# Optimization experiments

Hardware: AMD Instinct MI355X
Metric: run time of the kernel (lower is better)

The kernel has to match this reference:

```python
import jax, jax.numpy as jnp
import numpy as np

N, D, E = 50000, 128, 800000
EPS = 1e-5


def setup_inputs() -> dict:
    key = jax.random.key(0)
    ks = jax.random.split(key, 16)
    x = jax.random.normal(ks[0], (N, D), dtype=jnp.float32)
    edge_index = jax.random.randint(ks[1], (2, E), 0, N, dtype=jnp.int32)
    s = 1.0 / np.sqrt(D)
    inp = {"x": x, "edge_index": edge_index}
    for i in range(3):
        inp[f"lng{i}"] = jnp.ones((D,), jnp.float32)
        inp[f"lnb{i}"] = jnp.zeros((D,), jnp.float32)
        inp[f"W{i}"] = jax.random.normal(ks[2 + 2 * i], (D, D), jnp.float32) * s
        inp[f"b{i}"] = jnp.zeros((D,), jnp.float32)
    return inp


def _gcn_norm(edge_index):
    # PyG GCNConv default: add self loops, symmetric normalization D^-1/2 (A+I) D^-1/2
    loop = jnp.arange(N, dtype=edge_index.dtype)
    src = jnp.concatenate([edge_index[0], loop])  # [E+N]
    dst = jnp.concatenate([edge_index[1], loop])
    deg = jax.ops.segment_sum(jnp.ones_like(dst, jnp.float32), dst, num_segments=N)
    dinv = jnp.where(deg > 0, jax.lax.rsqrt(jnp.maximum(deg, 1.0)), 0.0)
    norm = dinv[src] * dinv[dst]  # [E+N]
    return src, dst, norm


def _layer(h, g, bt, W, b, src, dst, norm):
    # LayerNorm -> ReLU -> GCNConv
    mu = jnp.mean(h, axis=-1, keepdims=True)
    var = jnp.mean(jnp.square(h - mu), axis=-1, keepdims=True)
    hn = (h - mu) * jax.lax.rsqrt(var + EPS) * g + bt
    hn = jax.nn.relu(hn) @ W  # [N, D]
    msg = norm[:, None] * hn[src]  # [E+N, D] gather
    return jax.ops.segment_sum(msg, dst, num_segments=N) + b


def reference(x, edge_index, lng0, lnb0, W0, b0, lng1, lnb1, W1, b1, lng2, lnb2, W2, b2):
    src, dst, norm = _gcn_norm(edge_index)
    # conv0 (GCNLayer) + residual
    x = _layer(x, lng0, lnb0, W0, b0, src, dst, norm) + x
    # conv1 (ResGCNLayer: two GCNLayers) + residual
    h = _layer(x, lng1, lnb1, W1, b1, src, dst, norm)
    h = _layer(h, lng2, lnb2, W2, b2, src, dst, norm)
    return h + x
```

## Files before the change

### kernel.cpp

```cpp
#include <hip/hip_runtime.h>

#define N_NODES 50000
#define DIM     128
#define E_EDGES 800000
#define ELLW    64

typedef __attribute__((ext_vector_type(8))) short short8;
typedef __attribute__((ext_vector_type(4))) float f32x4;

__device__ __forceinline__ float bflo(unsigned int u){ return __uint_as_float(u << 16); }
__device__ __forceinline__ float bfhi(unsigned int u){ return __uint_as_float(u & 0xFFFF0000u); }
__device__ __forceinline__ unsigned int f2bf(float f){
  unsigned int u = __float_as_uint(f);
  return (u + 0x7FFFu + ((u >> 16) & 1u)) >> 16;
}
__device__ __forceinline__ unsigned int pack2(float a, float b){
  return f2bf(a) | (f2bf(b) << 16);
}


__global__ __launch_bounds__(256) void count_kernel(const int* __restrict__ edges,
                                                    int* __restrict__ cnt,
                                                    int* __restrict__ epos){
  int e = blockIdx.x * 256 + threadIdx.x;
  if (e < E_EDGES) epos[e] = atomicAdd(&cnt[edges[E_EDGES + e]], 1);
}

__global__ __launch_bounds__(256) void fill_kernel(const int* __restrict__ edges,
                                                   const int* __restrict__ epos,
                                                   const int* __restrict__ cnt,
                                                   int2* __restrict__ ell){
  int e = blockIdx.x * 256 + threadIdx.x;
  if (e < E_EDGES){
    int s = edges[e];
    int d = edges[E_EDGES + e];
    int pos = epos[e];
    if (pos < ELLW){
      float w = rsqrtf((float)(cnt[s] + 1)) * rsqrtf((float)(cnt[d] + 1));
      int2 pk; pk.x = s; pk.y = __float_as_int(w);
      ell[(size_t)d * ELLW + pos] = pk;
    }
  }
}

__global__ __launch_bounds__(256) void cvtw_all(const float* __restrict__ W0,
                                                const float* __restrict__ W1,
                                                const float* __restrict__ W2,
                                                unsigned short* __restrict__ Wt){
  int idx = blockIdx.x * 256 + threadIdx.x;
  int w = idx >> 14, r = idx & 16383;
  const float* W = (w == 0) ? W0 : (w == 1) ? W1 : W2;
  int k = r >> 7, n = r & 127;
  Wt[w * 16384 + n * 128 + k] = (unsigned short)f2bf(W[r]);
}


__global__ __launch_bounds__(256) void gemm_ln_mfma(const float* __restrict__ X,
                                                    const float* __restrict__ g,
                                                    const float* __restrict__ bt,
                                                    const unsigned short* __restrict__ Wt,
                                                    unsigned short* __restrict__ Y){
  __shared__ unsigned short ldsb[128 * 136];
  int tid = threadIdx.x;
  #pragma unroll
  for (int it = 0; it < 8; ++it){
    int c  = tid + it * 256;
    int n  = c >> 4, kc = c & 15;
    *(short8*)&ldsb[n * 136 + kc * 8] = *(const short8*)(Wt + n * 128 + kc * 8);
  }
  int wave = tid >> 6, lane = tid & 63, quad = lane >> 4, l15 = lane & 15;
  int rowbase = blockIdx.x * 128 + wave * 32;
  int rm0 = rowbase + l15;      if (rm0 > N_NODES - 1) rm0 = N_NODES - 1;
  int rm1 = rowbase + 16 + l15; if (rm1 > N_NODES - 1) rm1 = N_NODES - 1;

  float v0[4][8], v1[4][8];
  float s0 = 0.f, ss0 = 0.f, s1 = 0.f, ss1 = 0.f;
  #pragma unroll
  for (int kk = 0; kk < 4; ++kk){
    float4 xa = *(const float4*)(X + (size_t)rm0 * 128 + kk * 32 + quad * 8);
    float4 xb = *(const float4*)(X + (size_t)rm0 * 128 + kk * 32 + quad * 8 + 4);
    float4 ya = *(const float4*)(X + (size_t)rm1 * 128 + kk * 32 + quad * 8);
    float4 yb_ = *(const float4*)(X + (size_t)rm1 * 128 + kk * 32 + quad * 8 + 4);
    v0[kk][0]=xa.x; v0[kk][1]=xa.y; v0[kk][2]=xa.z; v0[kk][3]=xa.w;
    v0[kk][4]=xb.x; v0[kk][5]=xb.y; v0[kk][6]=xb.z; v0[kk][7]=xb.w;
    v1[kk][0]=ya.x; v1[kk][1]=ya.y; v1[kk][2]=ya.z; v1[kk][3]=ya.w;
    v1[kk][4]=yb_.x; v1[kk][5]=yb_.y; v1[kk][6]=yb_.z; v1[kk][7]=yb_.w;
    #pragma unroll
    for (int j = 0; j < 8; ++j){
      s0 += v0[kk][j]; ss0 += v0[kk][j] * v0[kk][j];
      s1 += v1[kk][j]; ss1 += v1[kk][j] * v1[kk][j];
    }
  }
  s0 += __shfl_xor(s0, 16, 64); ss0 += __shfl_xor(ss0, 16, 64);
  s0 += __shfl_xor(s0, 32, 64); ss0 += __shfl_xor(ss0, 32, 64);
  s1 += __shfl_xor(s1, 16, 64); ss1 += __shfl_xor(ss1, 16, 64);
  s1 += __shfl_xor(s1, 32, 64); ss1 += __shfl_xor(ss1, 32, 64);
  float mu0 = s0 * (1.0f/128.0f), var0 = ss0 * (1.0f/128.0f) - mu0*mu0;
  float mu1 = s1 * (1.0f/128.0f), var1 = ss1 * (1.0f/128.0f) - mu1*mu1;
  float rs0 = rsqrtf(var0 + 1e-5f), rs1 = rsqrtf(var1 + 1e-5f);

  short8 a0[4], a1[4];
  #pragma unroll
  for (int kk = 0; kk < 4; ++kk){
    float4 ga = *(const float4*)(g  + kk * 32 + quad * 8);
    float4 gb = *(const float4*)(g  + kk * 32 + quad * 8 + 4);
    float4 ba = *(const float4*)(bt + kk * 32 + quad * 8);
    float4 bb = *(const float4*)(bt + kk * 32 + quad * 8 + 4);
    float gg[8] = {ga.x,ga.y,ga.z,ga.w,gb.x,gb.y,gb.z,gb.w};
    float bbv[8] = {ba.x,ba.y,ba.z,ba.w,bb.x,bb.y,bb.z,bb.w};
    #pragma unroll
    for (int j = 0; j < 8; ++j){
      float h0 = fmaxf((v0[kk][j] - mu0) * rs0 * gg[j] + bbv[j], 0.0f);
      float h1 = fmaxf((v1[kk][j] - mu1) * rs1 * gg[j] + bbv[j], 0.0f);
      a0[kk][j] = (short)f2bf(h0);
      a1[kk][j] = (short)f2bf(h1);
    }
  }

  f32x4 acc[2][8];
  #pragma unroll
  for (int mt = 0; mt < 2; ++mt)
    #pragma unroll
    for (int nt = 0; nt < 8; ++nt) acc[mt][nt] = (f32x4){0.f, 0.f, 0.f, 0.f};
  __syncthreads();
  #pragma unroll
  for (int kk = 0; kk < 4; ++kk){
    #pragma unroll
    for (int nt = 0; nt < 8; ++nt){
      short8 b = *(const short8*)&ldsb[(nt * 16 + l15) * 136 + kk * 32 + quad * 8];
      acc[0][nt] = __builtin_amdgcn_mfma_f32_16x16x32_bf16(a0[kk], b, acc[0][nt], 0, 0, 0);
      acc[1][nt] = __builtin_amdgcn_mfma_f32_16x16x32_bf16(a1[kk], b, acc[1][nt], 0, 0, 0);
    }
  }
  #pragma unroll
  for (int mt = 0; mt < 2; ++mt)
    #pragma unroll
    for (int nt = 0; nt < 8; ++nt)
      #pragma unroll
      for (int r = 0; r < 4; ++r){
        int row = rowbase + mt * 16 + quad * 4 + r;
        if (row < N_NODES)
          Y[(size_t)row * 128 + nt * 16 + l15] = (unsigned short)f2bf(acc[mt][nt][r]);
      }
}


__global__ __launch_bounds__(256) void gemm_mfma(const unsigned short* __restrict__ A,
                                                 const unsigned short* __restrict__ Wt,
                                                 unsigned short* __restrict__ Y){
  __shared__ unsigned short ldsb[128 * 136];
  int tid = threadIdx.x;
  #pragma unroll
  for (int it = 0; it < 8; ++it){
    int c  = tid + it * 256;
    int n  = c >> 4, kc = c & 15;
    *(short8*)&ldsb[n * 136 + kc * 8] = *(const short8*)(Wt + n * 128 + kc * 8);
  }
  int wave = tid >> 6, lane = tid & 63, quad = lane >> 4, l15 = lane & 15;
  int rowbase = blockIdx.x * 128 + wave * 32;
  int rm0 = rowbase + l15;      if (rm0 > N_NODES - 1) rm0 = N_NODES - 1;
  int rm1 = rowbase + 16 + l15; if (rm1 > N_NODES - 1) rm1 = N_NODES - 1;

  short8 a0[4], a1[4];
  #pragma unroll
  for (int kk = 0; kk < 4; ++kk){
    a0[kk] = *(const short8*)(A + (size_t)rm0 * 128 + kk * 32 + quad * 8);
    a1[kk] = *(const short8*)(A + (size_t)rm1 * 128 + kk * 32 + quad * 8);
  }
  f32x4 acc[2][8];
  #pragma unroll
  for (int mt = 0; mt < 2; ++mt)
    #pragma unroll
    for (int nt = 0; nt < 8; ++nt) acc[mt][nt] = (f32x4){0.f, 0.f, 0.f, 0.f};
  __syncthreads();
  #pragma unroll
  for (int kk = 0; kk < 4; ++kk){
    #pragma unroll
    for (int nt = 0; nt < 8; ++nt){
      short8 b = *(const short8*)&ldsb[(nt * 16 + l15) * 136 + kk * 32 + quad * 8];
      acc[0][nt] = __builtin_amdgcn_mfma_f32_16x16x32_bf16(a0[kk], b, acc[0][nt], 0, 0, 0);
      acc[1][nt] = __builtin_amdgcn_mfma_f32_16x16x32_bf16(a1[kk], b, acc[1][nt], 0, 0, 0);
    }
  }
  #pragma unroll
  for (int mt = 0; mt < 2; ++mt)
    #pragma unroll
    for (int nt = 0; nt < 8; ++nt)
      #pragma unroll
      for (int r = 0; r < 4; ++r){
        int row = rowbase + mt * 16 + quad * 4 + r;
        if (row < N_NODES)
          Y[(size_t)row * 128 + nt * 16 + l15] = (unsigned short)f2bf(acc[mt][nt][r]);
      }
}


template<bool HAS_RES, bool DO_LN>
__global__ __launch_bounds__(256) void agg_kernel(const unsigned short* __restrict__ y,
                                                  const int* __restrict__ cnt,
                                                  const int2* __restrict__ ell,
                                                  const float* __restrict__ bias,
                                                  const float* __restrict__ res,
                                                  float* __restrict__ outp,
                                                  const float* __restrict__ lng,
                                                  const float* __restrict__ lnb,
                                                  unsigned short* __restrict__ hn_out){
  int wv   = (blockIdx.x * 256 + threadIdx.x) >> 6;
  int lane = threadIdx.x & 63;
  int hl   = lane & 15;
  int node = wv * 4 + (lane >> 4);
  int selbase = lane & 48;
  const uint4* y4 = (const uint4*)y;

  int deg = cnt[node];
  float di = rsqrtf((float)(deg + 1));
  float ws = di * di;

  const int2* row = ell + (size_t)node * ELLW;
  int2 e0 = row[hl], e1 = row[hl + 16], e2 = row[hl + 32], e3 = row[hl + 48];

  int J = deg;
  J = max(J, __shfl_xor(J, 16, 64));
  J = max(J, __shfl_xor(J, 32, 64));

  uint4 us = y4[(size_t)node * 16 + hl];
  float acc0 = ws * bflo(us.x), acc1 = ws * bfhi(us.x);
  float acc2 = ws * bflo(us.y), acc3 = ws * bfhi(us.y);
  float acc4 = ws * bflo(us.z), acc5 = ws * bfhi(us.z);
  float acc6 = ws * bflo(us.w), acc7 = ws * bfhi(us.w);

  auto block16 = [&](int2 ee, int base16){
    int rem = J - base16;
    if (rem <= 0) return;
    int nch = (min(rem, 16) + 3) >> 2;
    for (int c = 0; c < nch; ++c){
      int rb = c * 4;
      int sA = __shfl(ee.x, selbase | (rb + 0), 64);
      int sB = __shfl(ee.x, selbase | (rb + 1), 64);
      int sC = __shfl(ee.x, selbase | (rb + 2), 64);
      int sD = __shfl(ee.x, selbase | (rb + 3), 64);
      float wA = __uint_as_float((unsigned)__shfl(ee.y, selbase | (rb + 0), 64));
      float wB = __uint_as_float((unsigned)__shfl(ee.y, selbase | (rb + 1), 64));
      float wC = __uint_as_float((unsigned)__shfl(ee.y, selbase | (rb + 2), 64));
      float wD = __uint_as_float((unsigned)__shfl(ee.y, selbase | (rb + 3), 64));
      uint4 gA = y4[(size_t)sA * 16 + hl];
      uint4 gB = y4[(size_t)sB * 16 + hl];
      uint4 gC = y4[(size_t)sC * 16 + hl];
      uint4 gD = y4[(size_t)sD * 16 + hl];
      acc0 += wA*bflo(gA.x); acc1 += wA*bfhi(gA.x); acc2 += wA*bflo(gA.y); acc3 += wA*bfhi(gA.y);
      acc4 += wA*bflo(gA.z); acc5 += wA*bfhi(gA.z); acc6 += wA*bflo(gA.w); acc7 += wA*bfhi(gA.w);
      acc0 += wB*bflo(gB.x); acc1 += wB*bfhi(gB.x); acc2 += wB*bflo(gB.y); acc3 += wB*bfhi(gB.y);
      acc4 += wB*bflo(gB.z); acc5 += wB*bfhi(gB.z); acc6 += wB*bflo(gB.w); acc7 += wB*bfhi(gB.w);
      acc0 += wC*bflo(gC.x); acc1 += wC*bfhi(gC.x); acc2 += wC*bflo(gC.y); acc3 += wC*bfhi(gC.y);
      acc4 += wC*bflo(gC.z); acc5 += wC*bfhi(gC.z); acc6 += wC*bflo(gC.w); acc7 += wC*bfhi(gC.w);
      acc0 += wD*bflo(gD.x); acc1 += wD*bfhi(gD.x); acc2 += wD*bflo(gD.y); acc3 += wD*bfhi(gD.y);
      acc4 += wD*bflo(gD.z); acc5 += wD*bfhi(gD.z); acc6 += wD*bflo(gD.w); acc7 += wD*bfhi(gD.w);
    }
  };
  block16(e0, 0); block16(e1, 16); block16(e2, 32); block16(e3, 48);

  float4 ubA = ((const float4*)bias)[hl * 2];
  float4 ubB = ((const float4*)bias)[hl * 2 + 1];
  acc0 += ubA.x; acc1 += ubA.y; acc2 += ubA.z; acc3 += ubA.w;
  acc4 += ubB.x; acc5 += ubB.y; acc6 += ubB.z; acc7 += ubB.w;
  if (HAS_RES){
    float4 urA = ((const float4*)res)[(size_t)node * 32 + hl * 2];
    float4 urB = ((const float4*)res)[(size_t)node * 32 + hl * 2 + 1];
    acc0 += urA.x; acc1 += urA.y; acc2 += urA.z; acc3 += urA.w;
    acc4 += urB.x; acc5 += urB.y; acc6 += urB.z; acc7 += urB.w;
  }
  if (outp){
    float4 oA; oA.x = acc0; oA.y = acc1; oA.z = acc2; oA.w = acc3;
    float4 oB; oB.x = acc4; oB.y = acc5; oB.z = acc6; oB.w = acc7;
    ((float4*)outp)[(size_t)node * 32 + hl * 2]     = oA;
    ((float4*)outp)[(size_t)node * 32 + hl * 2 + 1] = oB;
  }

  if (DO_LN){
    float s  = acc0 + acc1 + acc2 + acc3 + acc4 + acc5 + acc6 + acc7;
    float ss = acc0*acc0 + acc1*acc1 + acc2*acc2 + acc3*acc3
             + acc4*acc4 + acc5*acc5 + acc6*acc6 + acc7*acc7;
    #pragma unroll
    for (int d = 8; d >= 1; d >>= 1){ s += __shfl_xor(s, d, 64); ss += __shfl_xor(ss, d, 64); }
    float mu  = s * (1.0f / 128.0f);
    float var = ss * (1.0f / 128.0f) - mu * mu;
    float rs  = rsqrtf(var + 1e-5f);
    float4 ugA = ((const float4*)lng)[hl * 2];
    float4 ugB = ((const float4*)lng)[hl * 2 + 1];
    float4 ubbA = ((const float4*)lnb)[hl * 2];
    float4 ubbB = ((const float4*)lnb)[hl * 2 + 1];
    float h0 = fmaxf((acc0 - mu) * rs * ugA.x + ubbA.x, 0.0f);
    float h1 = fmaxf((acc1 - mu) * rs * ugA.y + ubbA.y, 0.0f);
    float h2 = fmaxf((acc2 - mu) * rs * ugA.z + ubbA.z, 0.0f);
    float h3 = fmaxf((acc3 - mu) * rs * ugA.w + ubbA.w, 0.0f);
    float h4 = fmaxf((acc4 - mu) * rs * ugB.x + ubbB.x, 0.0f);
    float h5 = fmaxf((acc5 - mu) * rs * ugB.y + ubbB.y, 0.0f);
    float h6 = fmaxf((acc6 - mu) * rs * ugB.z + ubbB.z, 0.0f);
    float h7 = fmaxf((acc7 - mu) * rs * ugB.w + ubbB.w, 0.0f);
    uint4 ho;
    ho.x = pack2(h0, h1); ho.y = pack2(h2, h3);
    ho.z = pack2(h4, h5); ho.w = pack2(h6, h7);
    ((uint4*)hn_out)[(size_t)node * 16 + hl] = ho;
  }
}


extern "C" void kernel_launch(void* const* d_in, const int* in_sizes, int n_in,
                              void* d_out, int out_size, void* d_ws, size_t ws_size,
                              hipStream_t stream){
  const float* x    = (const float*)d_in[0];
  const int*   edges= (const int*)d_in[1];
  const float* lng0 = (const float*)d_in[2];
  const float* lnb0 = (const float*)d_in[3];
  const float* W0   = (const float*)d_in[4];
  const float* b0   = (const float*)d_in[5];
  const float* lng1 = (const float*)d_in[6];
  const float* lnb1 = (const float*)d_in[7];
  const float* W1   = (const float*)d_in[8];
  const float* b1   = (const float*)d_in[9];
  const float* lng2 = (const float*)d_in[10];
  const float* lnb2 = (const float*)d_in[11];
  const float* W2   = (const float*)d_in[12];
  const float* b2   = (const float*)d_in[13];

  char* p = (char*)d_ws;
  auto carve = [&](size_t bytes) -> void* {
    void* r = (void*)p;
    p += (bytes + 255) & ~(size_t)255;
    return r;
  };
  int*   cnt   = (int*)  carve(N_NODES * 4);
  int2*  ell   = (int2*) carve((size_t)N_NODES * ELLW * 8);
  size_t zspan = (char*)(ell + (size_t)N_NODES * ELLW) - (char*)cnt;
  int*   epos  = (int*)  carve((size_t)E_EDGES * 4);
  unsigned short* Wt = (unsigned short*)carve(3 * 128 * 128 * 2);
  unsigned short* hn = (unsigned short*)carve((size_t)N_NODES * 128 * 2);
  unsigned short* yb = (unsigned short*)carve((size_t)N_NODES * 128 * 2);
  float* out = (float*)d_out;

  hipMemsetAsync(cnt, 0, zspan, stream);

  count_kernel<<<(E_EDGES + 255) / 256, 256, 0, stream>>>(edges, cnt, epos);
  fill_kernel<<<(E_EDGES + 255) / 256, 256, 0, stream>>>(edges, epos, cnt, ell);
  cvtw_all<<<192, 256, 0, stream>>>(W0, W1, W2, Wt);

  const int GEMM_GRID = (N_NODES + 127) / 128;
  const int AGG_GRID  = N_NODES / 4 / 4;

  gemm_ln_mfma<<<GEMM_GRID, 256, 0, stream>>>(x, lng0, lnb0, Wt, yb);
  agg_kernel<true, true><<<AGG_GRID, 256, 0, stream>>>(yb, cnt, ell,
                                                       b0, x, out, lng1, lnb1, hn);
  gemm_mfma<<<GEMM_GRID, 256, 0, stream>>>(hn, Wt + 16384, yb);
  agg_kernel<false, true><<<AGG_GRID, 256, 0, stream>>>(yb, cnt, ell,
                                                        b1, nullptr, nullptr, lng2, lnb2, hn);
  gemm_mfma<<<GEMM_GRID, 256, 0, stream>>>(hn, Wt + 32768, yb);
  agg_kernel<true, false><<<AGG_GRID, 256, 0, stream>>>(yb, cnt, ell,
                                                        b2, out, out, nullptr, nullptr, nullptr);
}
```

Baseline: 300.3 us.

## Fuse all GCN stages into one persistent cooperative kernel with grid syncs

```diff
diff --git a/kernel.cpp b/kernel.cpp
--- a/kernel.cpp
+++ b/kernel.cpp
@@ -1,4 +1,7 @@
 #include <hip/hip_runtime.h>
+#include <hip/hip_cooperative_groups.h>
+
+namespace cg = cooperative_groups;
 
 #define N_NODES 50000
 #define DIM     128
@@ -18,310 +21,329 @@
   return f2bf(a) | (f2bf(b) << 16);
 }
 
-
-__global__ __launch_bounds__(256) void count_kernel(const int* __restrict__ edges,
-                                                    int* __restrict__ cnt,
-                                                    int* __restrict__ epos){
-  int e = blockIdx.x * 256 + threadIdx.x;
-  if (e < E_EDGES) epos[e] = atomicAdd(&cnt[edges[E_EDGES + e]], 1);
-}
-
-__global__ __launch_bounds__(256) void fill_kernel(const int* __restrict__ edges,
-                                                   const int* __restrict__ epos,
-                                                   const int* __restrict__ cnt,
-                                                   int2* __restrict__ ell){
-  int e = blockIdx.x * 256 + threadIdx.x;
-  if (e < E_EDGES){
-    int s = edges[e];
-    int d = edges[E_EDGES + e];
-    int pos = epos[e];
-    if (pos < ELLW){
-      float w = rsqrtf((float)(cnt[s] + 1)) * rsqrtf((float)(cnt[d] + 1));
-      int2 pk; pk.x = s; pk.y = __float_as_int(w);
-      ell[(size_t)d * ELLW + pos] = pk;
-    }
-  }
-}
-
-__global__ __launch_bounds__(256) void cvtw_all(const float* __restrict__ W0,
-                                                const float* __restrict__ W1,
-                                                const float* __restrict__ W2,
-                                                unsigned short* __restrict__ Wt){
-  int idx = blockIdx.x * 256 + threadIdx.x;
-  int w = idx >> 14, r = idx & 16383;
-  const float* W = (w == 0) ? W0 : (w == 1) ? W1 : W2;
-  int k = r >> 7, n = r & 127;
-  Wt[w * 16384 + n * 128 + k] = (unsigned short)f2bf(W[r]);
-}
-
-
-__global__ __launch_bounds__(256) void gemm_ln_mfma(const float* __restrict__ X,
-                                                    const float* __restrict__ g,
-                                                    const float* __restrict__ bt,
-                                                    const unsigned short* __restrict__ Wt,
-                                                    unsigned short* __restrict__ Y){
-  __shared__ unsigned short ldsb[128 * 136];
-  int tid = threadIdx.x;
-  #pragma unroll
-  for (int it = 0; it < 8; ++it){
-    int c  = tid + it * 256;
-    int n  = c >> 4, kc = c & 15;
-    *(short8*)&ldsb[n * 136 + kc * 8] = *(const short8*)(Wt + n * 128 + kc * 8);
-  }
-  int wave = tid >> 6, lane = tid & 63, quad = lane >> 4, l15 = lane & 15;
-  int rowbase = blockIdx.x * 128 + wave * 32;
-  int rm0 = rowbase + l15;      if (rm0 > N_NODES - 1) rm0 = N_NODES - 1;
-  int rm1 = rowbase + 16 + l15; if (rm1 > N_NODES - 1) rm1 = N_NODES - 1;
-
-  float v0[4][8], v1[4][8];
-  float s0 = 0.f, ss0 = 0.f, s1 = 0.f, ss1 = 0.f;
+struct Params {
+  const float* x; const int* edges;
+  const float* lng0; const float* lnb0; const float* W0; const float* b0;
+  const float* lng1; const float* lnb1; const float* W1; const float* b1;
+  const float* lng2; const float* lnb2; const float* W2; const float* b2;
+  int* cnt; int* epos; int2* ell; unsigned short* Wt;
+  unsigned short* hn; unsigned short* yb; float* out;
+};
+
+__device__ __forceinline__ void gemm_tile(const unsigned short* __restrict__ A,
+                                          const unsigned short* __restrict__ ldsb,
+                                          unsigned short* __restrict__ Y,
+                                          int base, int wave, int quad, int l15){
+  int rbase = base + wave * 16;
+  int rm = rbase + l15; if (rm > N_NODES - 1) rm = N_NODES - 1;
+  short8 a[4];
+  #pragma unroll
+  for (int kk = 0; kk < 4; ++kk)
+    a[kk] = *(const short8*)(A + (size_t)rm * 128 + kk * 32 + quad * 8);
+  f32x4 acc[8];
+  #pragma unroll
+  for (int nt = 0; nt < 8; ++nt) acc[nt] = (f32x4){0.f, 0.f, 0.f, 0.f};
+  #pragma unroll
+  for (int kk = 0; kk < 4; ++kk)
+    #pragma unroll
+    for (int nt = 0; nt < 8; ++nt){
+      short8 b = *(const short8*)&ldsb[(nt * 16 + l15) * 136 + kk * 32 + quad * 8];
+      acc[nt] = __builtin_amdgcn_mfma_f32_16x16x32_bf16(a[kk], b, acc[nt], 0, 0, 0);
+    }
+  #pragma unroll
+  for (int nt = 0; nt < 8; ++nt)
+    #pragma unroll
+    for (int r = 0; r < 4; ++r){
+      int row = rbase + quad * 4 + r;
+      if (row < N_NODES)
+        Y[(size_t)row * 128 + nt * 16 + l15] = (unsigned short)f2bf(acc[nt][r]);
+    }
+}
+
+__device__ __forceinline__ void gemm_ln_tile(const float* __restrict__ X,
+                                             const float* __restrict__ g,
+                                             const float* __restrict__ bt,
+                                             const unsigned short* __restrict__ ldsb,
+                                             unsigned short* __restrict__ Y,
+                                             int base, int wave, int quad, int l15){
+  int rbase = base + wave * 16;
+  int rm = rbase + l15; if (rm > N_NODES - 1) rm = N_NODES - 1;
+  float v[4][8];
+  float s = 0.f, ss = 0.f;
   #pragma unroll
   for (int kk = 0; kk < 4; ++kk){
-    float4 xa = *(const float4*)(X + (size_t)rm0 * 128 + kk * 32 + quad * 8);
-    float4 xb = *(const float4*)(X + (size_t)rm0 * 128 + kk * 32 + quad * 8 + 4);
-    float4 ya = *(const float4*)(X + (size_t)rm1 * 128 + kk * 32 + quad * 8);
-    float4 yb_ = *(const float4*)(X + (size_t)rm1 * 128 + kk * 32 + quad * 8 + 4);
-    v0[kk][0]=xa.x; v0[kk][1]=xa.y; v0[kk][2]=xa.z; v0[kk][3]=xa.w;
-    v0[kk][4]=xb.x; v0[kk][5]=xb.y; v0[kk][6]=xb.z; v0[kk][7]=xb.w;
-    v1[kk][0]=ya.x; v1[kk][1]=ya.y; v1[kk][2]=ya.z; v1[kk][3]=ya.w;
-    v1[kk][4]=yb_.x; v1[kk][5]=yb_.y; v1[kk][6]=yb_.z; v1[kk][7]=yb_.w;
-    #pragma unroll
-    for (int j = 0; j < 8; ++j){
-      s0 += v0[kk][j]; ss0 += v0[kk][j] * v0[kk][j];
-      s1 += v1[kk][j]; ss1 += v1[kk][j] * v1[kk][j];
-    }
-  }
-  s0 += __shfl_xor(s0, 16, 64); ss0 += __shfl_xor(ss0, 16, 64);
-  s0 += __shfl_xor(s0, 32, 64); ss0 += __shfl_xor(ss0, 32, 64);
-  s1 += __shfl_xor(s1, 16, 64); ss1 += __shfl_xor(ss1, 16, 64);
-  s1 += __shfl_xor(s1, 32, 64); ss1 += __shfl_xor(ss1, 32, 64);
-  float mu0 = s0 * (1.0f/128.0f), var0 = ss0 * (1.0f/128.0f) - mu0*mu0;
-  float mu1 = s1 * (1.0f/128.0f), var1 = ss1 * (1.0f/128.0f) - mu1*mu1;
-  float rs0 = rsqrtf(var0 + 1e-5f), rs1 = rsqrtf(var1 + 1e-5f);
-
-  short8 a0[4], a1[4];
+    float4 xa = *(const float4*)(X + (size_t)rm * 128 + kk * 32 + quad * 8);
+    float4 xb = *(const float4*)(X + (size_t)rm * 128 + kk * 32 + quad * 8 + 4);
+    v[kk][0]=xa.x; v[kk][1]=xa.y; v[kk][2]=xa.z; v[kk][3]=xa.w;
+    v[kk][4]=xb.x; v[kk][5]=xb.y; v[kk][6]=xb.z; v[kk][7]=xb.w;
+    #pragma unroll
+    for (int j = 0; j < 8; ++j){ s += v[kk][j]; ss += v[kk][j] * v[kk][j]; }
+  }
+  s += __shfl_xor(s, 16, 64); ss += __shfl_xor(ss, 16, 64);
+  s += __shfl_xor(s, 32, 64); ss += __shfl_xor(ss, 32, 64);
+  float mu = s * (1.0f/128.0f), var = ss * (1.0f/128.0f) - mu * mu;
+  float rs = rsqrtf(var + 1e-5f);
+  short8 a[4];
   #pragma unroll
   for (int kk = 0; kk < 4; ++kk){
     float4 ga = *(const float4*)(g  + kk * 32 + quad * 8);
     float4 gb = *(const float4*)(g  + kk * 32 + quad * 8 + 4);
     float4 ba = *(const float4*)(bt + kk * 32 + quad * 8);
     float4 bb = *(const float4*)(bt + kk * 32 + quad * 8 + 4);
-    float gg[8] = {ga.x,ga.y,ga.z,ga.w,gb.x,gb.y,gb.z,gb.w};
+    float gg[8]  = {ga.x,ga.y,ga.z,ga.w,gb.x,gb.y,gb.z,gb.w};
     float bbv[8] = {ba.x,ba.y,ba.z,ba.w,bb.x,bb.y,bb.z,bb.w};
     #pragma unroll
     for (int j = 0; j < 8; ++j){
-      float h0 = fmaxf((v0[kk][j] - mu0) * rs0 * gg[j] + bbv[j], 0.0f);
-      float h1 = fmaxf((v1[kk][j] - mu1) * rs1 * gg[j] + bbv[j], 0.0f);
-      a0[kk][j] = (short)f2bf(h0);
-      a1[kk][j] = (short)f2bf(h1);
-    }
-  }
-
-  f32x4 acc[2][8];
-  #pragma unroll
-  for (int mt = 0; mt < 2; ++mt)
-    #pragma unroll
-    for (int nt = 0; nt < 8; ++nt) acc[mt][nt] = (f32x4){0.f, 0.f, 0.f, 0.f};
-  __syncthreads();
-  #pragma unroll
-  for (int kk = 0; kk < 4; ++kk){
+      float h = fmaxf((v[kk][j] - mu) * rs * gg[j] + bbv[j], 0.0f);
+      a[kk][j] = (short)f2bf(h);
+    }
+  }
+  f32x4 acc[8];
+  #pragma unroll
+  for (int nt = 0; nt < 8; ++nt) acc[nt] = (f32x4){0.f, 0.f, 0.f, 0.f};
+  #pragma unroll
+  for (int kk = 0; kk < 4; ++kk)
     #pragma unroll
     for (int nt = 0; nt < 8; ++nt){
       short8 b = *(const short8*)&ldsb[(nt * 16 + l15) * 136 + kk * 32 + quad * 8];
-      acc[0][nt] = __builtin_amdgcn_mfma_f32_16x16x32_bf16(a0[kk], b, acc[0][nt], 0, 0, 0);
-      acc[1][nt] = __builtin_amdgcn_mfma_f32_16x16x32_bf16(a1[kk], b, acc[1][nt], 0, 0, 0);
-    }
-  }
-  #pragma unroll
-  for (int mt = 0; mt < 2; ++mt)
-    #pragma unroll
-    for (int nt = 0; nt < 8; ++nt)
+      acc[nt] = __builtin_amdgcn_mfma_f32_16x16x32_bf16(a[kk], b, acc[nt], 0, 0, 0);
+    }
+  #pragma unroll
+  for (int nt = 0; nt < 8; ++nt)
+    #pragma unroll
+    for (int r = 0; r < 4; ++r){
+      int row = rbase + quad * 4 + r;
+      if (row < N_NODES)
+        Y[(size_t)row * 128 + nt * 16 + l15] = (unsigned short)f2bf(acc[nt][r]);
+    }
+}
+
+template<bool HAS_RES, bool DO_LN>
+__device__ __forceinline__ void agg_phase(const Params& P,
+                                          const unsigned short* __restrict__ y,
+                                          const float* __restrict__ bias,
+                                          const float* __restrict__ res,
+                                          float* __restrict__ outp,
+                                          const float* __restrict__ lng,
+                                          const float* __restrict__ lnb,
+                                          unsigned short* __restrict__ hn_out,
+                                          int GB){
+  int tid = threadIdx.x, lane = tid & 63, wave = tid >> 6;
+  int hl = lane & 15, selbase = lane & 48;
+  const uint4* y4 = (const uint4*)y;
+  for (int u = blockIdx.x; u < 3125; u += GB){
+    int node = u * 16 + wave * 4 + (lane >> 4);
+    int deg = P.cnt[node];
+    float di = rsqrtf((float)(deg + 1));
+    float ws = di * di;
+
+    const int2* row = P.ell + (size_t)node * ELLW;
+    int2 e0 = row[hl], e1 = row[hl + 16], e2 = row[hl + 32], e3 = row[hl + 48];
+
+    int J = deg;
+    J = max(J, __shfl_xor(J, 16, 64));
+    J = max(J, __shfl_xor(J, 32, 64));
+
+    uint4 us = y4[(size_t)node * 16 + hl];
+    float acc0 = ws * bflo(us.x), acc1 = ws * bfhi(us.x);
+    float acc2 = ws * bflo(us.y), acc3 = ws * bfhi(us.y);
+    float acc4 = ws * bflo(us.z), acc5 = ws * bfhi(us.z);
+    float acc6 = ws * bflo(us.w), acc7 = ws * bfhi(us.w);
+
+    auto block16 = [&](int2 ee, int base16){
+      int rem = J - base16;
+      if (rem <= 0) return;
+      int nch = (min(rem, 16) + 3) >> 2;
+      for (int c = 0; c < nch; ++c){
+        int rb = c * 4;
+        int sA = __shfl(ee.x, selbase | (rb + 0), 64);
+        int sB = __shfl(ee.x, selbase | (rb + 1), 64);
+        int sC = __shfl(ee.x, selbase | (rb + 2), 64);
+        int sD = __shfl(ee.x, selbase | (rb + 3), 64);
+        float wA = __uint_as_float((unsigned)__shfl(ee.y, selbase | (rb + 0), 64));
+        float wB = __uint_as_float((unsigned)__shfl(ee.y, selbase | (rb + 1), 64));
+        float wC = __uint_as_float((unsigned)__shfl(ee.y, selbase | (rb + 2), 64));
+        float wD = __uint_as_float((unsigned)__shfl(ee.y, selbase | (rb + 3), 64));
+        uint4 gA = y4[(size_t)sA * 16 + hl];
+        uint4 gB = y4[(size_t)sB * 16 + hl];
+        uint4 gC = y4[(size_t)sC * 16 + hl];
+        uint4 gD = y4[(size_t)sD * 16 + hl];
+        acc0 += wA*bflo(gA.x); acc1 += wA*bfhi(gA.x); acc2 += wA*bflo(gA.y); acc3 += wA*bfhi(gA.y);
+        acc4 += wA*bflo(gA.z); acc5 += wA*bfhi(gA.z); acc6 += wA*bflo(gA.w); acc7 += wA*bfhi(gA.w);
+        acc0 += wB*bflo(gB.x); acc1 += wB*bfhi(gB.x); acc2 += wB*bflo(gB.y); acc3 += wB*bfhi(gB.y);
+        acc4 += wB*bflo(gB.z); acc5 += wB*bfhi(gB.z); acc6 += wB*bflo(gB.w); acc7 += wB*bfhi(gB.w);
+        acc0 += wC*bflo(gC.x); acc1 += wC*bfhi(gC.x); acc2 += wC*bflo(gC.y); acc3 += wC*bfhi(gC.y);
+        acc4 += wC*bflo(gC.z); acc5 += wC*bfhi(gC.z); acc6 += wC*bflo(gC.w); acc7 += wC*bfhi(gC.w);
+        acc0 += wD*bflo(gD.x); acc1 += wD*bfhi(gD.x); acc2 += wD*bflo(gD.y); acc3 += wD*bfhi(gD.y);
+        acc4 += wD*bflo(gD.z); acc5 += wD*bfhi(gD.z); acc6 += wD*bflo(gD.w); acc7 += wD*bfhi(gD.w);
+      }
+    };
+    block16(e0, 0); block16(e1, 16); block16(e2, 32); block16(e3, 48);
+
+    float4 ubA = ((const float4*)bias)[hl * 2];
+    float4 ubB = ((const float4*)bias)[hl * 2 + 1];
+    acc0 += ubA.x; acc1 += ubA.y; acc2 += ubA.z; acc3 += ubA.w;
+    acc4 += ubB.x; acc5 += ubB.y; acc6 += ubB.z; acc7 += ubB.w;
+    if (HAS_RES){
+      float4 urA = ((const float4*)res)[(size_t)node * 32 + hl * 2];
+      float4 urB = ((const float4*)res)[(size_t)node * 32 + hl * 2 + 1];
+      acc0 += urA.x; acc1 += urA.y; acc2 += urA.z; acc3 += urA.w;
+      acc4 += urB.x; acc5 += urB.y; acc6 += urB.z; acc7 += urB.w;
+    }
+    if (outp){
+      float4 oA; oA.x = acc0; oA.y = acc1; oA.z = acc2; oA.w = acc3;
+      float4 oB; oB.x = acc4; oB.y = acc5; oB.z = acc6; oB.w = acc7;
+      ((float4*)outp)[(size_t)node * 32 + hl * 2]     = oA;
+      ((float4*)outp)[(size_t)node * 32 + hl * 2 + 1] = oB;
+    }
+    if (DO_LN){
+      float s  = acc0 + acc1 + acc2 + acc3 + acc4 + acc5 + acc6 + acc7;
+      float ss = acc0*acc0 + acc1*acc1 + acc2*acc2 + acc3*acc3
+               + acc4*acc4 + acc5*acc5 + acc6*acc6 + acc7*acc7;
       #pragma unroll
-      for (int r = 0; r < 4; ++r){
-        int row = rowbase + mt * 16 + quad * 4 + r;
-        if (row < N_NODES)
-          Y[(size_t)row * 128 + nt * 16 + l15] = (unsigned short)f2bf(acc[mt][nt][r]);
+      for (int d = 8; d >= 1; d >>= 1){ s += __shfl_xor(s, d, 64); ss += __shfl_xor(ss, d, 64); }
+      float mu  = s * (1.0f / 128.0f);
+      float var = ss * (1.0f / 128.0f) - mu * mu;
+      float rs  = rsqrtf(var + 1e-5f);
+      float4 ugA = ((const float4*)lng)[hl * 2];
+      float4 ugB = ((const float4*)lng)[hl * 2 + 1];
+      float4 ubbA = ((const float4*)lnb)[hl * 2];
+      float4 ubbB = ((const float4*)lnb)[hl * 2 + 1];
+      float h0 = fmaxf((acc0 - mu) * rs * ugA.x + ubbA.x, 0.0f);
+      float h1 = fmaxf((acc1 - mu) * rs * ugA.y + ubbA.y, 0.0f);
+      float h2 = fmaxf((acc2 - mu) * rs * ugA.z + ubbA.z, 0.0f);
+      float h3 = fmaxf((acc3 - mu) * rs * ugA.w + ubbA.w, 0.0f);
+      float h4 = fmaxf((acc4 - mu) * rs * ugB.x + ubbB.x, 0.0f);
+      float h5 = fmaxf((acc5 - mu) * rs * ugB.y + ubbB.y, 0.0f);
+      float h6 = fmaxf((acc6 - mu) * rs * ugB.z + ubbB.z, 0.0f);
+      float h7 = fmaxf((acc7 - mu) * rs * ugB.w + ubbB.w, 0.0f);
+      uint4 ho;
+      ho.x = pack2(h0, h1); ho.y = pack2(h2, h3);
+      ho.z = pack2(h4, h5); ho.w = pack2(h6, h7);
+      ((uint4*)hn_out)[(size_t)node * 16 + hl] = ho;
+    }
+  }
+}
+
+
+__global__ __launch_bounds__(256, 4) void mono_kernel(Params P){
+  cg::grid_group grid = cg::this_grid();
+  __shared__ unsigned short ldsb[128 * 136];
+  const int GB   = gridDim.x;
+  const int tid  = threadIdx.x;
+  const int wave = tid >> 6, lane = tid & 63;
+  const int quad = lane >> 4, l15 = lane & 15;
+
+  for (int u = blockIdx.x; u < 196; u += GB){
+    int i = u * 256 + tid;
+    if (i < N_NODES) P.cnt[i] = 0;
+  }
+  grid.sync();
+
+  {
+    const int NU_CNT = 3125, NU_CVT = 192;
+    for (int u = blockIdx.x; u < NU_CNT + NU_CVT; u += GB){
+      if (u < NU_CNT){
+        int e = u * 256 + tid;
+        if (e < E_EDGES) P.epos[e] = atomicAdd(&P.cnt[P.edges[E_EDGES + e]], 1);
+      } else {
+        int idx = (u - NU_CNT) * 256 + tid;
+        int w = idx >> 14, r = idx & 16383;
+        const float* W = (w == 0) ? P.W0 : (w == 1) ? P.W1 : P.W2;
+        P.Wt[w * 16384 + (r & 127) * 128 + (r >> 7)] = (unsigned short)f2bf(W[r]);
       }
-}
-
-
-__global__ __launch_bounds__(256) void gemm_mfma(const unsigned short* __restrict__ A,
-                                                 const unsigned short* __restrict__ Wt,
-                                                 unsigned short* __restrict__ Y){
-  __shared__ unsigned short ldsb[128 * 136];
-  int tid = threadIdx.x;
-  #pragma unroll
-  for (int it = 0; it < 8; ++it){
-    int c  = tid + it * 256;
-    int n  = c >> 4, kc = c & 15;
-    *(short8*)&ldsb[n * 136 + kc * 8] = *(const short8*)(Wt + n * 128 + kc * 8);
-  }
-  int wave = tid >> 6, lane = tid & 63, quad = lane >> 4, l15 = lane & 15;
-  int rowbase = blockIdx.x * 128 + wave * 32;
-  int rm0 = rowbase + l15;      if (rm0 > N_NODES - 1) rm0 = N_NODES - 1;
-  int rm1 = rowbase + 16 + l15; if (rm1 > N_NODES - 1) rm1 = N_NODES - 1;
-
-  short8 a0[4], a1[4];
-  #pragma unroll
-  for (int kk = 0; kk < 4; ++kk){
-    a0[kk] = *(const short8*)(A + (size_t)rm0 * 128 + kk * 32 + quad * 8);
-    a1[kk] = *(const short8*)(A + (size_t)rm1 * 128 + kk * 32 + quad * 8);
-  }
-  f32x4 acc[2][8];
-  #pragma unroll
-  for (int mt = 0; mt < 2; ++mt)
-    #pragma unroll
-    for (int nt = 0; nt < 8; ++nt) acc[mt][nt] = (f32x4){0.f, 0.f, 0.f, 0.f};
-  __syncthreads();
-  #pragma unroll
-  for (int kk = 0; kk < 4; ++kk){
-    #pragma unroll
-    for (int nt = 0; nt < 8; ++nt){
-      short8 b = *(const short8*)&ldsb[(nt * 16 + l15) * 136 + kk * 32 + quad * 8];
-      acc[0][nt] = __builtin_amdgcn_mfma_f32_16x16x32_bf16(a0[kk], b, acc[0][nt], 0, 0, 0);
-      acc[1][nt] = __builtin_amdgcn_mfma_f32_16x16x32_bf16(a1[kk], b, acc[1][nt], 0, 0, 0);
-    }
-  }
-  #pragma unroll
-  for (int mt = 0; mt < 2; ++mt)
-    #pragma unroll
-    for (int nt = 0; nt < 8; ++nt)
-      #pragma unroll
-      for (int r = 0; r < 4; ++r){
-        int row = rowbase + mt * 16 + quad * 4 + r;
-        if (row < N_NODES)
-          Y[(size_t)row * 128 + nt * 16 + l15] = (unsigned short)f2bf(acc[mt][nt][r]);
+    }
+  }
+  grid.sync();
+
+  {
+    #pragma unroll
+    for (int it = 0; it < 8; ++it){
+      int c = tid + it * 256;
+      int n = c >> 4, kc = c & 15;
+      *(short8*)&ldsb[n * 136 + kc * 8] = *(const short8*)(P.Wt + n * 128 + kc * 8);
+    }
+    __syncthreads();
+    const int NU_FILL = 3125, NU_PAD = 196, NU_G = 782;
+    for (int u = blockIdx.x; u < NU_FILL + NU_PAD + NU_G; u += GB){
+      if (u < NU_FILL){
+        int e = u * 256 + tid;
+        if (e < E_EDGES){
+          int s = P.edges[e], d = P.edges[E_EDGES + e];
+          int pos = P.epos[e];
+          if (pos < ELLW){
+            float w = rsqrtf((float)(P.cnt[s] + 1)) * rsqrtf((float)(P.cnt[d] + 1));
+            int2 pk; pk.x = s; pk.y = __float_as_int(w);
+            P.ell[(size_t)d * ELLW + pos] = pk;
+          }
+        }
+      } else if (u < NU_FILL + NU_PAD){
+        int i = (u - NU_FILL) * 256 + tid;
+        if (i < N_NODES){
+          int deg = P.cnt[i];
+          int g4 = (i >> 2) << 2;
+          int J = max(max(P.cnt[g4], P.cnt[g4 + 1]), max(P.cnt[g4 + 2], P.cnt[g4 + 3]));
+          int J4 = min(ELLW, (J + 3) & ~3);
+          int2 z; z.x = 0; z.y = 0;
+          for (int pp = min(deg, J4); pp < J4; ++pp)
+            P.ell[(size_t)i * ELLW + pp] = z;
+        }
+      } else {
+        gemm_ln_tile(P.x, P.lng0, P.lnb0, ldsb, P.yb,
+                     (u - NU_FILL - NU_PAD) * 64, wave, quad, l15);
       }
-}
-
-
-template<bool HAS_RES, bool DO_LN>
-__global__ __launch_bounds__(256) void agg_kernel(const unsigned short* __restrict__ y,
-                                                  const int* __restrict__ cnt,
-                                                  const int2* __restrict__ ell,
-                                                  const float* __restrict__ bias,
-                                                  const float* __restrict__ res,
-                                                  float* __restrict__ outp,
-                                                  const float* __restrict__ lng,
-                                                  const float* __restrict__ lnb,
-                                                  unsigned short* __restrict__ hn_out){
-  int wv   = (blockIdx.x * 256 + threadIdx.x) >> 6;
-  int lane = threadIdx.x & 63;
-  int hl   = lane & 15;
-  int node = wv * 4 + (lane >> 4);
-  int selbase = lane & 48;
-  const uint4* y4 = (const uint4*)y;
-
-  int deg = cnt[node];
-  float di = rsqrtf((float)(deg + 1));
-  float ws = di * di;
-
-  const int2* row = ell + (size_t)node * ELLW;
-  int2 e0 = row[hl], e1 = row[hl + 16], e2 = row[hl + 32], e3 = row[hl + 48];
-
-  int J = deg;
-  J = max(J, __shfl_xor(J, 16, 64));
-  J = max(J, __shfl_xor(J, 32, 64));
-
-  uint4 us = y4[(size_t)node * 16 + hl];
-  float acc0 = ws * bflo(us.x), acc1 = ws * bfhi(us.x);
-  float acc2 = ws * bflo(us.y), acc3 = ws * bfhi(us.y);
-  float acc4 = ws * bflo(us.z), acc5 = ws * bfhi(us.z);
-  float acc6 = ws * bflo(us.w), acc7 = ws * bfhi(us.w);
-
-  auto block16 = [&](int2 ee, int base16){
-    int rem = J - base16;
-    if (rem <= 0) return;
-    int nch = (min(rem, 16) + 3) >> 2;
-    for (int c = 0; c < nch; ++c){
-      int rb = c * 4;
-      int sA = __shfl(ee.x, selbase | (rb + 0), 64);
-      int sB = __shfl(ee.x, selbase | (rb + 1), 64);
-      int sC = __shfl(ee.x, selbase | (rb + 2), 64);
-      int sD = __shfl(ee.x, selbase | (rb + 3), 64);
-      float wA = __uint_as_float((unsigned)__shfl(ee.y, selbase | (rb + 0), 64));
-      float wB = __uint_as_float((unsigned)__shfl(ee.y, selbase | (rb + 1), 64));
-      float wC = __uint_as_float((unsigned)__shfl(ee.y, selbase | (rb + 2), 64));
-      float wD = __uint_as_float((unsigned)__shfl(ee.y, selbase | (rb + 3), 64));
-      uint4 gA = y4[(size_t)sA * 16 + hl];
-      uint4 gB = y4[(size_t)sB * 16 + hl];
-      uint4 gC = y4[(size_t)sC * 16 + hl];
-      uint4 gD = y4[(size_t)sD * 16 + hl];
-      acc0 += wA*bflo(gA.x); acc1 += wA*bfhi(gA.x); acc2 += wA*bflo(gA.y); acc3 += wA*bfhi(gA.y);
-      acc4 += wA*bflo(gA.z); acc5 += wA*bfhi(gA.z); acc6 += wA*bflo(gA.w); acc7 += wA*bfhi(gA.w);
-      acc0 += wB*bflo(gB.x); acc1 += wB*bfhi(gB.x); acc2 += wB*bflo(gB.y); acc3 += wB*bfhi(gB.y);
-      acc4 += wB*bflo(gB.z); acc5 += wB*bfhi(gB.z); acc6 += wB*bflo(gB.w); acc7 += wB*bfhi(gB.w);
-      acc0 += wC*bflo(gC.x); acc1 += wC*bfhi(gC.x); acc2 += wC*bflo(gC.y); acc3 += wC*bfhi(gC.y);
-      acc4 += wC*bflo(gC.z); acc5 += wC*bfhi(gC.z); acc6 += wC*bflo(gC.w); acc7 += wC*bfhi(gC.w);
-      acc0 += wD*bflo(gD.x); acc1 += wD*bfhi(gD.x); acc2 += wD*bflo(gD.y); acc3 += wD*bfhi(gD.y);
-      acc4 += wD*bflo(gD.z); acc5 += wD*bfhi(gD.z); acc6 += wD*bflo(gD.w); acc7 += wD*bfhi(gD.w);
-    }
-  };
-  block16(e0, 0); block16(e1, 16); block16(e2, 32); block16(e3, 48);
-
-  float4 ubA = ((const float4*)bias)[hl * 2];
-  float4 ubB = ((const float4*)bias)[hl * 2 + 1];
-  acc0 += ubA.x; acc1 += ubA.y; acc2 += ubA.z; acc3 += ubA.w;
-  acc4 += ubB.x; acc5 += ubB.y; acc6 += ubB.z; acc7 += ubB.w;
-  if (HAS_RES){
-    float4 urA = ((const float4*)res)[(size_t)node * 32 + hl * 2];
-    float4 urB = ((const float4*)res)[(size_t)node * 32 + hl * 2 + 1];
-    acc0 += urA.x; acc1 += urA.y; acc2 += urA.z; acc3 += urA.w;
-    acc4 += urB.x; acc5 += urB.y; acc6 += urB.z; acc7 += urB.w;
-  }
-  if (outp){
-    float4 oA; oA.x = acc0; oA.y = acc1; oA.z = acc2; oA.w = acc3;
-    float4 oB; oB.x = acc4; oB.y = acc5; oB.z = acc6; oB.w = acc7;
-    ((float4*)outp)[(size_t)node * 32 + hl * 2]     = oA;
-    ((float4*)outp)[(size_t)node * 32 + hl * 2 + 1] = oB;
-  }
-
-  if (DO_LN){
-    float s  = acc0 + acc1 + acc2 + acc3 + acc4 + acc5 + acc6 + acc7;
-    float ss = acc0*acc0 + acc1*acc1 + acc2*acc2 + acc3*acc3
-             + acc4*acc4 + acc5*acc5 + acc6*acc6 + acc7*acc7;
-    #pragma unroll
-    for (int d = 8; d >= 1; d >>= 1){ s += __shfl_xor(s, d, 64); ss += __shfl_xor(ss, d, 64); }
-    float mu  = s * (1.0f / 128.0f);
-    float var = ss * (1.0f / 128.0f) - mu * mu;
-    float rs  = rsqrtf(var + 1e-5f);
-    float4 ugA = ((const float4*)lng)[hl * 2];
-    float4 ugB = ((const float4*)lng)[hl * 2 + 1];
-    float4 ubbA = ((const float4*)lnb)[hl * 2];
-    float4 ubbB = ((const float4*)lnb)[hl * 2 + 1];
-    float h0 = fmaxf((acc0 - mu) * rs * ugA.x + ubbA.x, 0.0f);
-    float h1 = fmaxf((acc1 - mu) * rs * ugA.y + ubbA.y, 0.0f);
-    float h2 = fmaxf((acc2 - mu) * rs * ugA.z + ubbA.z, 0.0f);
-    float h3 = fmaxf((acc3 - mu) * rs * ugA.w + ubbA.w, 0.0f);
-    float h4 = fmaxf((acc4 - mu) * rs * ugB.x + ubbB.x, 0.0f);
-    float h5 = fmaxf((acc5 - mu) * rs * ugB.y + ubbB.y, 0.0f);
-    float h6 = fmaxf((acc6 - mu) * rs * ugB.z + ubbB.z, 0.0f);
-    float h7 = fmaxf((acc7 - mu) * rs * ugB.w + ubbB.w, 0.0f);
-    uint4 ho;
-    ho.x = pack2(h0, h1); ho.y = pack2(h2, h3);
-    ho.z = pack2(h4, h5); ho.w = pack2(h6, h7);
-    ((uint4*)hn_out)[(size_t)node * 16 + hl] = ho;
-  }
+    }
+  }
+  grid.sync();
+
+  agg_phase<true, true>(P, P.yb, P.b0, P.x, P.out, P.lng1, P.lnb1, P.hn, GB);
+  grid.sync();
+
+  {
+    #pragma unroll
+    for (int it = 0; it < 8; ++it){
+      int c = tid + it * 256;
+      int n = c >> 4, kc = c & 15;
+      *(short8*)&ldsb[n * 136 + kc * 8] = *(const short8*)(P.Wt + 16384 + n * 128 + kc * 8);
+    }
+    __syncthreads();
+    for (int u = blockIdx.x; u < 782; u += GB)
+      gemm_tile(P.hn, ldsb, P.yb, u * 64, wave, quad, l15);
+  }
+  grid.sync();
+
+  agg_phase<false, true>(P, P.yb, P.b1, nullptr, nullptr, P.lng2, P.lnb2, P.hn, GB);
+  grid.sync();
+
+  {
+    #pragma unroll
+    for (int it = 0; it < 8; ++it){
+      int c = tid + it * 256;
+      int n = c >> 4, kc = c & 15;
+      *(short8*)&ldsb[n * 136 + kc * 8] = *(const short8*)(P.Wt + 32768 + n * 128 + kc * 8);
+    }
+    __syncthreads();
+    for (int u = blockIdx.x; u < 782; u += GB)
+      gemm_tile(P.hn, ldsb, P.yb, u * 64, wave, quad, l15);
+  }
+  grid.sync();
+
+  agg_phase<true, false>(P, P.yb, P.b2, P.out, P.out, nullptr, nullptr, nullptr, GB);
 }
 
 
 extern "C" void kernel_launch(void* const* d_in, const int* in_sizes, int n_in,
                               void* d_out, int out_size, void* d_ws, size_t ws_size,
                               hipStream_t stream){
-  const float* x    = (const float*)d_in[0];
-  const int*   edges= (const int*)d_in[1];
-  const float* lng0 = (const float*)d_in[2];
-  const float* lnb0 = (const float*)d_in[3];
-  const float* W0   = (const float*)d_in[4];
-  const float* b0   = (const float*)d_in[5];
-  const float* lng1 = (const float*)d_in[6];
-  const float* lnb1 = (const float*)d_in[7];
-  const float* W1   = (const float*)d_in[8];
-  const float* b1   = (const float*)d_in[9];
-  const float* lng2 = (const float*)d_in[10];
-  const float* lnb2 = (const float*)d_in[11];
-  const float* W2   = (const float*)d_in[12];
-  const float* b2   = (const float*)d_in[13];
+  Params P;
+  P.x    = (const float*)d_in[0];
+  P.edges= (const int*)d_in[1];
+  P.lng0 = (const float*)d_in[2];  P.lnb0 = (const float*)d_in[3];
+  P.W0   = (const float*)d_in[4];  P.b0   = (const float*)d_in[5];
+  P.lng1 = (const float*)d_in[6];  P.lnb1 = (const float*)d_in[7];
+  P.W1   = (const float*)d_in[8];  P.b1   = (const float*)d_in[9];
+  P.lng2 = (const float*)d_in[10]; P.lnb2 = (const float*)d_in[11];
+  P.W2   = (const float*)d_in[12]; P.b2   = (const float*)d_in[13];
 
   char* p = (char*)d_ws;
   auto carve = [&](size_t bytes) -> void* {
@@ -329,31 +351,23 @@
     p += (bytes + 255) & ~(size_t)255;
     return r;
   };
-  int*   cnt   = (int*)  carve(N_NODES * 4);
-  int2*  ell   = (int2*) carve((size_t)N_NODES * ELLW * 8);
-  size_t zspan = (char*)(ell + (size_t)N_NODES * ELLW) - (char*)cnt;
-  int*   epos  = (int*)  carve((size_t)E_EDGES * 4);
-  unsigned short* Wt = (unsigned short*)carve(3 * 128 * 128 * 2);
-  unsigned short* hn = (unsigned short*)carve((size_t)N_NODES * 128 * 2);
-  unsigned short* yb = (unsigned short*)carve((size_t)N_NODES * 128 * 2);
-  float* out = (float*)d_out;
-
-  hipMemsetAsync(cnt, 0, zspan, stream);
-
-  count_kernel<<<(E_EDGES + 255) / 256, 256, 0, stream>>>(edges, cnt, epos);
-  fill_kernel<<<(E_EDGES + 255) / 256, 256, 0, stream>>>(edges, epos, cnt, ell);
-  cvtw_all<<<192, 256, 0, stream>>>(W0, W1, W2, Wt);
-
-  const int GEMM_GRID = (N_NODES + 127) / 128;
-  const int AGG_GRID  = N_NODES / 4 / 4;
-
-  gemm_ln_mfma<<<GEMM_GRID, 256, 0, stream>>>(x, lng0, lnb0, Wt, yb);
-  agg_kernel<true, true><<<AGG_GRID, 256, 0, stream>>>(yb, cnt, ell,
-                                                       b0, x, out, lng1, lnb1, hn);
-  gemm_mfma<<<GEMM_GRID, 256, 0, stream>>>(hn, Wt + 16384, yb);
-  agg_kernel<false, true><<<AGG_GRID, 256, 0, stream>>>(yb, cnt, ell,
-                                                        b1, nullptr, nullptr, lng2, lnb2, hn);
-  gemm_mfma<<<GEMM_GRID, 256, 0, stream>>>(hn, Wt + 32768, yb);
-  agg_kernel<true, false><<<AGG_GRID, 256, 0, stream>>>(yb, cnt, ell,
-                                                        b2, out, out, nullptr, nullptr, nullptr);
-}
+  P.cnt  = (int*)  carve(N_NODES * 4);
+  P.epos = (int*)  carve((size_t)E_EDGES * 4);
+  P.ell  = (int2*) carve((size_t)N_NODES * ELLW * 8);
+  P.Wt   = (unsigned short*)carve(3 * 128 * 128 * 2);
+  P.hn   = (unsigned short*)carve((size_t)N_NODES * 128 * 2);
+  P.yb   = (unsigned short*)carve((size_t)N_NODES * 128 * 2);
+  P.out  = (float*)d_out;
+
+  int maxb = 0;
+  hipError_t oe = hipOccupancyMaxActiveBlocksPerMultiprocessor(&maxb, mono_kernel, 256, 0);
+  int ncu = 256;
+  int dev = 0;
+  hipGetDevice(&dev);
+  hipDeviceGetAttribute(&ncu, hipDeviceAttributeMultiprocessorCount, dev);
+  int GB = (oe == hipSuccess && maxb > 0) ? maxb * ncu : 2 * ncu;
+  if (GB > 3125) GB = 3125;
+
+  void* args[] = { (void*)&P };
+  hipLaunchCooperativeKernel(mono_kernel, dim3(GB), dim3(256), args, 0, stream);
+}
```

Measured after the change: 785.4 us. +161.6%, slower.
